# Performance work log

Measured on AMD Instinct MI355X. Metric: run time of the kernel, lower is better.

Reference implementation:

```python
import jax, jax.numpy as jnp
import numpy as np

HEAD_SIZE = 64
D_MODEL = 768


def setup_inputs() -> dict:
    key = jax.random.key(0)
    ks = jax.random.split(key, 7)
    x = jax.random.normal(ks[0], (8, 4096, D_MODEL), dtype=jnp.float32)
    def lin_init(kw, kb, fan_in, fan_out):
        bound = 1.0 / np.sqrt(fan_in)
        W = jax.random.uniform(kw, (fan_in, fan_out), minval=-bound, maxval=bound, dtype=jnp.float32)
        b = jax.random.uniform(kb, (fan_out,), minval=-bound, maxval=bound, dtype=jnp.float32)
        return W, b
    Wq, bq = lin_init(ks[1], ks[2], D_MODEL, HEAD_SIZE)
    Wk, bk = lin_init(ks[3], ks[4], D_MODEL, HEAD_SIZE)
    Wv, bv = lin_init(ks[5], ks[6], D_MODEL, HEAD_SIZE)
    return {"x": x, "Wq": Wq, "bq": bq, "Wk": Wk, "bk": bk, "Wv": Wv, "bv": bv}


def reference(x, Wq, bq, Wk, bk, Wv, bv):
    # x: [B, N, 768]; projections to [B, N, head_size]
    q = jnp.einsum("bnd,dh->bnh", x, Wq) + bq
    k = jnp.einsum("bnd,dh->bnh", x, Wk) + bk
    v = jnp.einsum("bnd,dh->bnh", x, Wv) + bv
    scale = 1.0 / jnp.sqrt(jnp.asarray(q.shape[-1], dtype=q.dtype))
    wei = jnp.einsum("bqh,bkh->bqk", q, k) * scale  # [B, N, N]
    wei = jax.nn.softmax(wei, axis=-1)
    out = jnp.einsum("bqk,bkh->bqh", wei, v)  # [B, N, head_size]
    return out
```

## Files before the change

kernel.cpp:

```cpp
#include <hip/hip_runtime.h>
#include <stdint.h>
#include <stddef.h>

typedef __bf16 bf16x8 __attribute__((ext_vector_type(8)));
typedef __bf16 bf16x4 __attribute__((ext_vector_type(4)));
typedef float  f32x4  __attribute__((ext_vector_type(4)));

#define MFMA16(A, B, C) __builtin_amdgcn_mfma_f32_16x16x32_bf16((A), (B), (C), 0, 0, 0)

#define QSCALE 0.18033688011112042f

#if __has_builtin(__builtin_amdgcn_exp2f)
__device__ __forceinline__ float fast_exp2(float x) {
    return __builtin_amdgcn_exp2f(x);
}
#else
__device__ __forceinline__ float fast_exp2(float x) {
    float r;
    asm("v_exp_f32 %0, %1" : "=v"(r) : "v"(x));
    return r;
}
#endif

__device__ __forceinline__ void async_copy16(__bf16* lds, const __bf16* g) {
    __builtin_amdgcn_global_load_lds(
        (const __attribute__((address_space(1))) void*)g,
        (__attribute__((address_space(3))) void*)lds,
        16, 0, 0);
}

__global__ __launch_bounds__(256) void qkv_proj_kernel(
    const float* __restrict__ x,
    const float* __restrict__ Wq, const float* __restrict__ bq,
    const float* __restrict__ Wk, const float* __restrict__ bk,
    const float* __restrict__ Wv, const float* __restrict__ bv,
    __bf16* __restrict__ Qg, __bf16* __restrict__ Kg, __bf16* __restrict__ Vpg)
{
    __shared__ __bf16 xs[64][40];
    __shared__ __bf16 wt[192][40];

    const int tid  = threadIdx.x;
    const int wid  = tid >> 6;
    const int lane = tid & 63;
    const int l15  = lane & 15;
    const int l4   = lane >> 4;
    const int m0   = blockIdx.x * 64;

    f32x4 acc[4][3];
    #pragma unroll
    for (int i = 0; i < 4; ++i)
        #pragma unroll
        for (int j = 0; j < 3; ++j)
            acc[i][j] = (f32x4){0.f, 0.f, 0.f, 0.f};

    for (int k0 = 0; k0 < 768; k0 += 32) {
        #pragma unroll
        for (int i = 0; i < 2; ++i) {
            int idx = tid + 256 * i;
            int row = idx >> 3;
            int c4  = idx & 7;
            const float4 v = *reinterpret_cast<const float4*>(
                x + (size_t)(m0 + row) * 768 + k0 + c4 * 4);
            bf16x4 t;
            t[0] = (__bf16)v.x; t[1] = (__bf16)v.y;
            t[2] = (__bf16)v.z; t[3] = (__bf16)v.w;
            *reinterpret_cast<bf16x4*>(&xs[row][c4 * 4]) = t;
        }
        #pragma unroll
        for (int i = 0; i < 6; ++i) {
            int idx = tid + 256 * i;
            int kg  = idx / 192;
            int c   = idx - kg * 192;
            const float* Wm = (c < 64) ? Wq : ((c < 128) ? Wk : Wv);
            int cc = c & 63;
            bf16x4 t;
            #pragma unroll
            for (int j = 0; j < 4; ++j)
                t[j] = (__bf16)Wm[(size_t)(k0 + kg * 4 + j) * 64 + cc];
            *reinterpret_cast<bf16x4*>(&wt[c][kg * 4]) = t;
        }
        __syncthreads();

        bf16x8 afrag[4];
        #pragma unroll
        for (int rf = 0; rf < 4; ++rf)
            afrag[rf] = *reinterpret_cast<const bf16x8*>(&xs[rf * 16 + l15][l4 * 8]);
        #pragma unroll
        for (int cf = 0; cf < 3; ++cf) {
            bf16x8 bfrag = *reinterpret_cast<const bf16x8*>(
                &wt[wid * 48 + cf * 16 + l15][l4 * 8]);
            #pragma unroll
            for (int rf = 0; rf < 4; ++rf)
                acc[rf][cf] = MFMA16(afrag[rf], bfrag, acc[rf][cf]);
        }
        __syncthreads();
    }

    #pragma unroll
    for (int cf = 0; cf < 3; ++cf) {
        int col = wid * 48 + cf * 16 + l15;
        int mi  = col >> 6;
        int h   = col & 63;
        float bias = (mi == 0) ? bq[h] : ((mi == 1) ? bk[h] : bv[h]);
        float scl  = (mi == 0) ? QSCALE : 1.0f;
        #pragma unroll
        for (int rf = 0; rf < 4; ++rf) {
            int r0 = rf * 16 + l4 * 4;
            if (mi == 2) {
                int m  = m0 + r0;
                int bb = m >> 12;
                int n0 = m & 4095;
                int n0p = (n0 & ~31) | (l4 * 8 + (rf & 1) * 4);
                bf16x4 t;
                #pragma unroll
                for (int r = 0; r < 4; ++r)
                    t[r] = (__bf16)(acc[rf][cf][r] + bias);
                *reinterpret_cast<bf16x4*>(
                    Vpg + ((size_t)bb * 64 + h) * 4096 + n0p) = t;
            } else {
                __bf16* G = (mi == 0) ? Qg : Kg;
                #pragma unroll
                for (int r = 0; r < 4; ++r)
                    G[(size_t)(m0 + r0 + r) * 64 + h] =
                        (__bf16)((acc[rf][cf][r] + bias) * scl);
            }
        }
    }
}

__global__ __launch_bounds__(512, 4) void attn_kernel(
    const __bf16* __restrict__ Qg, const __bf16* __restrict__ Kg,
    const __bf16* __restrict__ Vpg, float* __restrict__ out)
{
    __shared__ __align__(16) char smem[65536];
    __bf16* ksbase = reinterpret_cast<__bf16*>(smem);
    __bf16* vsbase = ksbase + 4 * 2 * 32 * 64;

    const int tid  = threadIdx.x;
    const int wid  = tid >> 6;
    const int lane = tid & 63;
    const int l15  = lane & 15;
    const int l4   = lane >> 4;
    const int qw2  = wid & 1;
    const int ks   = wid >> 1;
    const int b    = blockIdx.x & 7;
    const int qb   = blockIdx.x >> 3;
    const int q0   = qb * 64 + qw2 * 32;

    const __bf16* Kb = Kg  + (size_t)b * 4096 * 64;
    const __bf16* Vb = Vpg + (size_t)b * 64 * 4096;

    __bf16* kst0 = ksbase + (ks * 2 + 0) * 32 * 64;
    __bf16* kst1 = ksbase + (ks * 2 + 1) * 32 * 64;
    __bf16* vst0 = vsbase + (ks * 2 + 0) * 64 * 32;
    __bf16* vst1 = vsbase + (ks * 2 + 1) * 64 * 32;

    int koff[2][2], voff[4];
    #pragma unroll
    for (int dc = 0; dc < 2; ++dc)
        #pragma unroll
        for (int cf = 0; cf < 2; ++cf) {
            int row = cf * 16 + l15;
            koff[dc][cf] = row * 64 + (((dc * 4 + l4) ^ (row & 7)) * 8);
        }
    #pragma unroll
    for (int ht = 0; ht < 4; ++ht) {
        int row = ht * 16 + l15;
        voff[ht] = row * 32 + ((l4 ^ (row & 3)) * 8);
    }

    const int krow_s = qw2 * 16 + (lane >> 3);
    const int kg_s   = (lane & 7) ^ (lane >> 3);
    const int vrow_s = qw2 * 32 + (lane >> 2);
    const int vg_s   = (lane & 3) ^ ((lane >> 2) & 3);

    auto issue_stage = [&](__bf16* kp, __bf16* vp, int c) {
        #pragma unroll
        for (int j = 0; j < 2; ++j) {
            async_copy16(kp + (qw2 * 16 + j * 8) * 64,
                         Kb + (size_t)(c * 32 + krow_s + j * 8) * 64 + kg_s * 8);
            async_copy16(vp + (qw2 * 32 + j * 16) * 32,
                         Vb + (size_t)(vrow_s + j * 16) * 4096 + c * 32 + vg_s * 8);
        }
    };

    bf16x8 aq[2][2];
    #pragma unroll
    for (int set = 0; set < 2; ++set)
        #pragma unroll
        for (int dc = 0; dc < 2; ++dc)
            aq[set][dc] = *reinterpret_cast<const bf16x8*>(
                Qg + (size_t)(b * 4096 + q0 + set * 16 + l15) * 64 + dc * 32 + l4 * 8);

    f32x4 lacc0 = (f32x4){0.f, 0.f, 0.f, 0.f};
    f32x4 lacc1 = (f32x4){0.f, 0.f, 0.f, 0.f};
    f32x4 o[2][4];
    #pragma unroll
    for (int set = 0; set < 2; ++set)
        #pragma unroll
        for (int ht = 0; ht < 4; ++ht)
            o[set][ht] = (f32x4){0.f, 0.f, 0.f, 0.f};

    const int c0 = ks * 32;
    issue_stage(kst0, vst0, c0);

    for (int t = 0; t < 32; ++t) {
        __syncthreads();
        const __bf16* kp = (t & 1) ? kst1 : kst0;
        const __bf16* vp = (t & 1) ? vst1 : vst0;
        __bf16* kpn = (t & 1) ? kst0 : kst1;
        __bf16* vpn = (t & 1) ? vst0 : vst1;
        const bool pre = (t + 1) < 32;
        if (pre) issue_stage(kpn, vpn, c0 + t + 1);

        f32x4 s0[2], s1[2];
        #pragma unroll
        for (int cf = 0; cf < 2; ++cf) {
            s0[cf] = (f32x4){0.f, 0.f, 0.f, 0.f};
            s1[cf] = (f32x4){0.f, 0.f, 0.f, 0.f};
        }
        __builtin_amdgcn_s_setprio(1);
        #pragma unroll
        for (int dc = 0; dc < 2; ++dc)
            #pragma unroll
            for (int cf = 0; cf < 2; ++cf) {
                bf16x8 kf = *reinterpret_cast<const bf16x8*>(kp + koff[dc][cf]);
                s0[cf] = MFMA16(kf, aq[0][dc], s0[cf]);
                s1[cf] = MFMA16(kf, aq[1][dc], s1[cf]);
            }
        __builtin_amdgcn_s_setprio(0);

        #pragma unroll
        for (int cf = 0; cf < 2; ++cf)
            #pragma unroll
            for (int r = 0; r < 4; ++r) {
                s0[cf][r] = fast_exp2(s0[cf][r]);
                s1[cf][r] = fast_exp2(s1[cf][r]);
            }
        lacc0 += s0[0]; lacc0 += s0[1];
        lacc1 += s1[0]; lacc1 += s1[1];

        bf16x8 pb0, pb1;
        #pragma unroll
        for (int j = 0; j < 4; ++j) {
            pb0[j]     = (__bf16)s0[0][j];
            pb0[j + 4] = (__bf16)s0[1][j];
            pb1[j]     = (__bf16)s1[0][j];
            pb1[j + 4] = (__bf16)s1[1][j];
        }

        __builtin_amdgcn_s_setprio(1);
        #pragma unroll
        for (int ht = 0; ht < 4; ++ht) {
            bf16x8 vf = *reinterpret_cast<const bf16x8*>(vp + voff[ht]);
            o[0][ht] = MFMA16(vf, pb0, o[0][ht]);
            o[1][ht] = MFMA16(vf, pb1, o[1][ht]);
        }
        __builtin_amdgcn_s_setprio(0);
    }

    float l0 = lacc0[0] + lacc0[1] + lacc0[2] + lacc0[3];
    float l1 = lacc1[0] + lacc1[1] + lacc1[2] + lacc1[3];
    l0 += __shfl_xor(l0, 16); l0 += __shfl_xor(l0, 32);
    l1 += __shfl_xor(l1, 16); l1 += __shfl_xor(l1, 32);

    __syncthreads();
    float* lbuf = reinterpret_cast<float*>(smem);
    float* smO  = lbuf + 256;

    if (l4 == 0) {
        lbuf[((qw2 * 2 + 0) * 4 + ks) * 16 + l15] = l0;
        lbuf[((qw2 * 2 + 1) * 4 + ks) * 16 + l15] = l1;
    }
    const int hcol = 4 * l4;
    if (ks != 0) {
        #pragma unroll
        for (int set = 0; set < 2; ++set)
            #pragma unroll
            for (int ht = 0; ht < 4; ++ht)
                *reinterpret_cast<f32x4*>(
                    &smO[(((ks - 1) * 2 + qw2) * 32 + set * 16 + l15) * 68
                         + ht * 16 + hcol]) = o[set][ht];
    }
    __syncthreads();
    if (ks == 0) {
        #pragma unroll
        for (int set = 0; set < 2; ++set) {
            float L = lbuf[((qw2 * 2 + set) * 4 + 0) * 16 + l15]
                    + lbuf[((qw2 * 2 + set) * 4 + 1) * 16 + l15]
                    + lbuf[((qw2 * 2 + set) * 4 + 2) * 16 + l15]
                    + lbuf[((qw2 * 2 + set) * 4 + 3) * 16 + l15];
            float inv = 1.0f / L;
            #pragma unroll
            for (int ht = 0; ht < 4; ++ht) {
                f32x4 acc = o[set][ht];
                #pragma unroll
                for (int k = 1; k < 4; ++k) {
                    f32x4 p = *reinterpret_cast<const f32x4*>(
                        &smO[(((k - 1) * 2 + qw2) * 32 + set * 16 + l15) * 68
                             + ht * 16 + hcol]);
                    acc[0] += p[0]; acc[1] += p[1]; acc[2] += p[2]; acc[3] += p[3];
                }
                acc[0] *= inv; acc[1] *= inv; acc[2] *= inv; acc[3] *= inv;
                *reinterpret_cast<f32x4*>(
                    out + (size_t)(b * 4096 + q0 + set * 16 + l15) * 64
                        + ht * 16 + hcol) = acc;
            }
        }
    }
}

extern "C" void kernel_launch(void* const* d_in, const int* in_sizes, int n_in,
                              void* d_out, int out_size, void* d_ws, size_t ws_size,
                              hipStream_t stream)
{
    (void)in_sizes; (void)n_in; (void)out_size; (void)ws_size;
    const float* x  = (const float*)d_in[0];
    const float* Wq = (const float*)d_in[1];
    const float* bq = (const float*)d_in[2];
    const float* Wk = (const float*)d_in[3];
    const float* bk = (const float*)d_in[4];
    const float* Wv = (const float*)d_in[5];
    const float* bv = (const float*)d_in[6];
    float* out = (float*)d_out;

    __bf16* Qg  = (__bf16*)d_ws;
    __bf16* Kg  = Qg + (size_t)32768 * 64;
    __bf16* Vpg = Kg + (size_t)32768 * 64;

    qkv_proj_kernel<<<512, 256, 0, stream>>>(x, Wq, bq, Wk, bk, Wv, bv, Qg, Kg, Vpg);
    attn_kernel<<<512, 512, 0, stream>>>(Qg, Kg, Vpg, out);
}
```

Baseline: 75.54 us.

## Load V fragments directly from global into registers instead of LDS staging

V tiles are no longer staged through shared memory with async copies. Each lane now loads its V fragments straight from global memory into registers one iteration ahead, double-buffered in registers, and the loop is unrolled by two so the buffers can swap statically. Shared memory per block shrinks, which removes LDS traffic and bank pressure for V. In exchange it adds register pressure and relies on the global load latency being hidden within one iteration, with no coalescing help from LDS.

```diff
diff --git a/kernel.cpp b/kernel.cpp
--- a/kernel.cpp
+++ b/kernel.cpp
@@ -132,9 +132,8 @@
     const __bf16* __restrict__ Qg, const __bf16* __restrict__ Kg,
     const __bf16* __restrict__ Vpg, float* __restrict__ out)
 {
-    __shared__ __align__(16) char smem[65536];
+    __shared__ __align__(16) char smem[53248];
     __bf16* ksbase = reinterpret_cast<__bf16*>(smem);
-    __bf16* vsbase = ksbase + 4 * 2 * 32 * 64;
 
     const int tid  = threadIdx.x;
     const int wid  = tid >> 6;
@@ -152,10 +151,8 @@
 
     __bf16* kst0 = ksbase + (ks * 2 + 0) * 32 * 64;
     __bf16* kst1 = ksbase + (ks * 2 + 1) * 32 * 64;
-    __bf16* vst0 = vsbase + (ks * 2 + 0) * 64 * 32;
-    __bf16* vst1 = vsbase + (ks * 2 + 1) * 64 * 32;
-
-    int koff[2][2], voff[4];
+
+    int koff[2][2];
     #pragma unroll
     for (int dc = 0; dc < 2; ++dc)
         #pragma unroll
@@ -163,25 +160,22 @@
             int row = cf * 16 + l15;
             koff[dc][cf] = row * 64 + (((dc * 4 + l4) ^ (row & 7)) * 8);
         }
-    #pragma unroll
-    for (int ht = 0; ht < 4; ++ht) {
-        int row = ht * 16 + l15;
-        voff[ht] = row * 32 + ((l4 ^ (row & 3)) * 8);
-    }
 
     const int krow_s = qw2 * 16 + (lane >> 3);
     const int kg_s   = (lane & 7) ^ (lane >> 3);
-    const int vrow_s = qw2 * 32 + (lane >> 2);
-    const int vg_s   = (lane & 3) ^ ((lane >> 2) & 3);
-
-    auto issue_stage = [&](__bf16* kp, __bf16* vp, int c) {
-        #pragma unroll
-        for (int j = 0; j < 2; ++j) {
+
+    auto issue_stageK = [&](__bf16* kp, int c) {
+        #pragma unroll
+        for (int j = 0; j < 2; ++j)
             async_copy16(kp + (qw2 * 16 + j * 8) * 64,
                          Kb + (size_t)(c * 32 + krow_s + j * 8) * 64 + kg_s * 8);
-            async_copy16(vp + (qw2 * 32 + j * 16) * 32,
-                         Vb + (size_t)(vrow_s + j * 16) * 4096 + c * 32 + vg_s * 8);
-        }
+    };
+
+    auto vloadR = [&](bf16x8 (&dst)[4], int c) {
+        #pragma unroll
+        for (int ht = 0; ht < 4; ++ht)
+            dst[ht] = *reinterpret_cast<const bf16x8*>(
+                Vb + (size_t)(ht * 16 + l15) * 4096 + c * 32 + l4 * 8);
     };
 
     bf16x8 aq[2][2];
@@ -202,16 +196,17 @@
             o[set][ht] = (f32x4){0.f, 0.f, 0.f, 0.f};
 
     const int c0 = ks * 32;
-    issue_stage(kst0, vst0, c0);
-
-    for (int t = 0; t < 32; ++t) {
+
+    bf16x8 va[4], vb_[4];
+
+    auto body = [&](int t, const __bf16* kp, __bf16* kpn,
+                    bf16x8 (&vcur)[4], bf16x8 (&vnxt)[4]) {
         __syncthreads();
-        const __bf16* kp = (t & 1) ? kst1 : kst0;
-        const __bf16* vp = (t & 1) ? vst1 : vst0;
-        __bf16* kpn = (t & 1) ? kst0 : kst1;
-        __bf16* vpn = (t & 1) ? vst0 : vst1;
         const bool pre = (t + 1) < 32;
-        if (pre) issue_stage(kpn, vpn, c0 + t + 1);
+        if (pre) {
+            issue_stageK(kpn, c0 + t + 1);
+            vloadR(vnxt, c0 + t + 1);
+        }
 
         f32x4 s0[2], s1[2];
         #pragma unroll
@@ -224,9 +219,9 @@
         for (int dc = 0; dc < 2; ++dc)
             #pragma unroll
             for (int cf = 0; cf < 2; ++cf) {
-                bf16x8 kf = *reinterpret_cast<const bf16x8*>(kp + koff[dc][cf]);
-                s0[cf] = MFMA16(kf, aq[0][dc], s0[cf]);
-                s1[cf] = MFMA16(kf, aq[1][dc], s1[cf]);
+                bf16x8 kfr = *reinterpret_cast<const bf16x8*>(kp + koff[dc][cf]);
+                s0[cf] = MFMA16(kfr, aq[0][dc], s0[cf]);
+                s1[cf] = MFMA16(kfr, aq[1][dc], s1[cf]);
             }
         __builtin_amdgcn_s_setprio(0);
 
@@ -252,11 +247,18 @@
         __builtin_amdgcn_s_setprio(1);
         #pragma unroll
         for (int ht = 0; ht < 4; ++ht) {
-            bf16x8 vf = *reinterpret_cast<const bf16x8*>(vp + voff[ht]);
-            o[0][ht] = MFMA16(vf, pb0, o[0][ht]);
-            o[1][ht] = MFMA16(vf, pb1, o[1][ht]);
+            o[0][ht] = MFMA16(vcur[ht], pb0, o[0][ht]);
+            o[1][ht] = MFMA16(vcur[ht], pb1, o[1][ht]);
         }
         __builtin_amdgcn_s_setprio(0);
+    };
+
+    issue_stageK(kst0, c0);
+    vloadR(va, c0);
+
+    for (int j = 0; j < 16; ++j) {
+        body(2 * j,     kst0, kst1, va,  vb_);
+        body(2 * j + 1, kst1, kst0, vb_, va);
     }
 
     float l0 = lacc0[0] + lacc0[1] + lacc0[2] + lacc0[3];
```

Measured after the change: 130.6 us. 1.73x slower.

## Split attention key range across two blocks with separate merge kernel

Applied to the files above, without the earlier changes.

Splits each query tile's key range in half across two blocks, doubling the grid to 1024 blocks. Partial unnormalized outputs and row sums go to workspace, and a new merge kernel combines and normalizes them. Shared memory is halved by dropping double buffering, and the cross-wave reduction now reuses one buffer serially, so more blocks can fit per CU. In exchange it adds an extra kernel launch, global round-trips for the partials, and loses the overlap of loads with compute.

```diff
diff --git a/kernel.cpp b/kernel.cpp
--- a/kernel.cpp
+++ b/kernel.cpp
@@ -128,13 +128,14 @@
     }
 }
 
-__global__ __launch_bounds__(512, 4) void attn_kernel(
+__global__ __launch_bounds__(512, 8) void attn_kernel(
     const __bf16* __restrict__ Qg, const __bf16* __restrict__ Kg,
-    const __bf16* __restrict__ Vpg, float* __restrict__ out)
+    const __bf16* __restrict__ Vpg, float* __restrict__ po,
+    float* __restrict__ pl)
 {
-    __shared__ __align__(16) char smem[65536];
+    __shared__ __align__(16) char smem[32768];
     __bf16* ksbase = reinterpret_cast<__bf16*>(smem);
-    __bf16* vsbase = ksbase + 4 * 2 * 32 * 64;
+    __bf16* vsbase = ksbase + 4 * 32 * 64;
 
     const int tid  = threadIdx.x;
     const int wid  = tid >> 6;
@@ -144,16 +145,16 @@
     const int qw2  = wid & 1;
     const int ks   = wid >> 1;
     const int b    = blockIdx.x & 7;
-    const int qb   = blockIdx.x >> 3;
+    const int idx  = blockIdx.x >> 3;
+    const int qb   = idx & 63;
+    const int half = idx >> 6;
     const int q0   = qb * 64 + qw2 * 32;
 
     const __bf16* Kb = Kg  + (size_t)b * 4096 * 64;
     const __bf16* Vb = Vpg + (size_t)b * 64 * 4096;
 
-    __bf16* kst0 = ksbase + (ks * 2 + 0) * 32 * 64;
-    __bf16* kst1 = ksbase + (ks * 2 + 1) * 32 * 64;
-    __bf16* vst0 = vsbase + (ks * 2 + 0) * 64 * 32;
-    __bf16* vst1 = vsbase + (ks * 2 + 1) * 64 * 32;
+    __bf16* kst = ksbase + ks * 32 * 64;
+    __bf16* vst = vsbase + ks * 64 * 32;
 
     int koff[2][2], voff[4];
     #pragma unroll
@@ -174,12 +175,12 @@
     const int vrow_s = qw2 * 32 + (lane >> 2);
     const int vg_s   = (lane & 3) ^ ((lane >> 2) & 3);
 
-    auto issue_stage = [&](__bf16* kp, __bf16* vp, int c) {
+    auto issue_stage = [&](int c) {
         #pragma unroll
         for (int j = 0; j < 2; ++j) {
-            async_copy16(kp + (qw2 * 16 + j * 8) * 64,
+            async_copy16(kst + (qw2 * 16 + j * 8) * 64,
                          Kb + (size_t)(c * 32 + krow_s + j * 8) * 64 + kg_s * 8);
-            async_copy16(vp + (qw2 * 32 + j * 16) * 32,
+            async_copy16(vst + (qw2 * 32 + j * 16) * 32,
                          Vb + (size_t)(vrow_s + j * 16) * 4096 + c * 32 + vg_s * 8);
         }
     };
@@ -201,17 +202,11 @@
         for (int ht = 0; ht < 4; ++ht)
             o[set][ht] = (f32x4){0.f, 0.f, 0.f, 0.f};
 
-    const int c0 = ks * 32;
-    issue_stage(kst0, vst0, c0);
-
-    for (int t = 0; t < 32; ++t) {
-        __syncthreads();
-        const __bf16* kp = (t & 1) ? kst1 : kst0;
-        const __bf16* vp = (t & 1) ? vst1 : vst0;
-        __bf16* kpn = (t & 1) ? kst0 : kst1;
-        __bf16* vpn = (t & 1) ? vst0 : vst1;
-        const bool pre = (t + 1) < 32;
-        if (pre) issue_stage(kpn, vpn, c0 + t + 1);
+    const int c0 = half * 64 + ks * 16;
+
+    for (int t = 0; t < 16; ++t) {
+        issue_stage(c0 + t);
+        __syncthreads();
 
         f32x4 s0[2], s1[2];
         #pragma unroll
@@ -224,7 +219,7 @@
         for (int dc = 0; dc < 2; ++dc)
             #pragma unroll
             for (int cf = 0; cf < 2; ++cf) {
-                bf16x8 kf = *reinterpret_cast<const bf16x8*>(kp + koff[dc][cf]);
+                bf16x8 kf = *reinterpret_cast<const bf16x8*>(kst + koff[dc][cf]);
                 s0[cf] = MFMA16(kf, aq[0][dc], s0[cf]);
                 s1[cf] = MFMA16(kf, aq[1][dc], s1[cf]);
             }
@@ -252,11 +247,13 @@
         __builtin_amdgcn_s_setprio(1);
         #pragma unroll
         for (int ht = 0; ht < 4; ++ht) {
-            bf16x8 vf = *reinterpret_cast<const bf16x8*>(vp + voff[ht]);
+            bf16x8 vf = *reinterpret_cast<const bf16x8*>(vst + voff[ht]);
             o[0][ht] = MFMA16(vf, pb0, o[0][ht]);
             o[1][ht] = MFMA16(vf, pb1, o[1][ht]);
         }
         __builtin_amdgcn_s_setprio(0);
+
+        __syncthreads();
     }
 
     float l0 = lacc0[0] + lacc0[1] + lacc0[2] + lacc0[3];
@@ -264,50 +261,77 @@
     l0 += __shfl_xor(l0, 16); l0 += __shfl_xor(l0, 32);
     l1 += __shfl_xor(l1, 16); l1 += __shfl_xor(l1, 32);
 
-    __syncthreads();
     float* lbuf = reinterpret_cast<float*>(smem);
-    float* smO  = lbuf + 256;
+    float* smO2 = lbuf + 256;
 
     if (l4 == 0) {
         lbuf[((qw2 * 2 + 0) * 4 + ks) * 16 + l15] = l0;
         lbuf[((qw2 * 2 + 1) * 4 + ks) * 16 + l15] = l1;
     }
     const int hcol = 4 * l4;
-    if (ks != 0) {
-        #pragma unroll
-        for (int set = 0; set < 2; ++set)
+    #pragma unroll
+    for (int k = 1; k < 4; ++k) {
+        if (ks == k) {
+            #pragma unroll
+            for (int set = 0; set < 2; ++set)
+                #pragma unroll
+                for (int ht = 0; ht < 4; ++ht)
+                    *reinterpret_cast<f32x4*>(
+                        &smO2[(qw2 * 32 + set * 16 + l15) * 68 + ht * 16 + hcol]) =
+                        o[set][ht];
+        }
+        __syncthreads();
+        if (ks == 0) {
+            #pragma unroll
+            for (int set = 0; set < 2; ++set)
+                #pragma unroll
+                for (int ht = 0; ht < 4; ++ht) {
+                    f32x4 p = *reinterpret_cast<const f32x4*>(
+                        &smO2[(qw2 * 32 + set * 16 + l15) * 68 + ht * 16 + hcol]);
+                    o[set][ht][0] += p[0]; o[set][ht][1] += p[1];
+                    o[set][ht][2] += p[2]; o[set][ht][3] += p[3];
+                }
+        }
+        __syncthreads();
+    }
+
+    if (ks == 0) {
+        float* pop = po + (size_t)half * 32768 * 64;
+        #pragma unroll
+        for (int set = 0; set < 2; ++set) {
+            int row = b * 4096 + q0 + set * 16 + l15;
             #pragma unroll
             for (int ht = 0; ht < 4; ++ht)
                 *reinterpret_cast<f32x4*>(
-                    &smO[(((ks - 1) * 2 + qw2) * 32 + set * 16 + l15) * 68
-                         + ht * 16 + hcol]) = o[set][ht];
-    }
-    __syncthreads();
-    if (ks == 0) {
-        #pragma unroll
-        for (int set = 0; set < 2; ++set) {
-            float L = lbuf[((qw2 * 2 + set) * 4 + 0) * 16 + l15]
-                    + lbuf[((qw2 * 2 + set) * 4 + 1) * 16 + l15]
-                    + lbuf[((qw2 * 2 + set) * 4 + 2) * 16 + l15]
-                    + lbuf[((qw2 * 2 + set) * 4 + 3) * 16 + l15];
-            float inv = 1.0f / L;
-            #pragma unroll
-            for (int ht = 0; ht < 4; ++ht) {
-                f32x4 acc = o[set][ht];
-                #pragma unroll
-                for (int k = 1; k < 4; ++k) {
-                    f32x4 p = *reinterpret_cast<const f32x4*>(
-                        &smO[(((k - 1) * 2 + qw2) * 32 + set * 16 + l15) * 68
-                             + ht * 16 + hcol]);
-                    acc[0] += p[0]; acc[1] += p[1]; acc[2] += p[2]; acc[3] += p[3];
-                }
-                acc[0] *= inv; acc[1] *= inv; acc[2] *= inv; acc[3] *= inv;
-                *reinterpret_cast<f32x4*>(
-                    out + (size_t)(b * 4096 + q0 + set * 16 + l15) * 64
-                        + ht * 16 + hcol) = acc;
+                    pop + (size_t)row * 64 + ht * 16 + hcol) = o[set][ht];
+            if (l4 == 0) {
+                float L = lbuf[((qw2 * 2 + set) * 4 + 0) * 16 + l15]
+                        + lbuf[((qw2 * 2 + set) * 4 + 1) * 16 + l15]
+                        + lbuf[((qw2 * 2 + set) * 4 + 2) * 16 + l15]
+                        + lbuf[((qw2 * 2 + set) * 4 + 3) * 16 + l15];
+                pl[half * 32768 + row] = L;
             }
         }
     }
+}
+
+__global__ __launch_bounds__(256) void merge_kernel(
+    const float* __restrict__ po, const float* __restrict__ pl,
+    float* __restrict__ out)
+{
+    int gid = blockIdx.x * 256 + threadIdx.x;
+    int row = gid >> 4;
+    int c4  = (gid & 15) * 4;
+    float inv = 1.0f / (pl[row] + pl[32768 + row]);
+    const float4 a = *reinterpret_cast<const float4*>(po + (size_t)row * 64 + c4);
+    const float4 b = *reinterpret_cast<const float4*>(
+        po + (size_t)(32768 + row) * 64 + c4);
+    float4 r;
+    r.x = (a.x + b.x) * inv;
+    r.y = (a.y + b.y) * inv;
+    r.z = (a.z + b.z) * inv;
+    r.w = (a.w + b.w) * inv;
+    *reinterpret_cast<float4*>(out + (size_t)row * 64 + c4) = r;
 }
 
 extern "C" void kernel_launch(void* const* d_in, const int* in_sizes, int n_in,
@@ -327,7 +351,10 @@
     __bf16* Qg  = (__bf16*)d_ws;
     __bf16* Kg  = Qg + (size_t)32768 * 64;
     __bf16* Vpg = Kg + (size_t)32768 * 64;
+    float*  po  = (float*)(Vpg + (size_t)32768 * 64);
+    float*  pl  = po + (size_t)2 * 32768 * 64;
 
     qkv_proj_kernel<<<512, 256, 0, stream>>>(x, Wq, bq, Wk, bk, Wv, bv, Qg, Kg, Vpg);
-    attn_kernel<<<512, 512, 0, stream>>>(Qg, Kg, Vpg, out);
-}
+    attn_kernel<<<1024, 512, 0, stream>>>(Qg, Kg, Vpg, po, pl);
+    merge_kernel<<<2048, 256, 0, stream>>>(po, pl, out);
+}
```

Result: slower. 243.6 us (+222.5%).

## Give each wave all 64 queries and split keys eight ways with tree reduction

Applied to the files above, without the earlier changes.

Each wave now covers all 64 queries of the block instead of 32, and the key range is split across eight waves instead of four. Every K/V fragment read from LDS therefore feeds four MFMAs instead of two, which cuts LDS read traffic per unit of math. Each wave also copies whole 32-key stages on its own. The partial outputs are combined with a three-level tree reduction through LDS. In exchange, LDS use doubles to 128 KB per block and per-wave registers grow, so fewer blocks can be resident per CU and latency hiding may suffer.

```diff
diff --git a/kernel.cpp b/kernel.cpp
--- a/kernel.cpp
+++ b/kernel.cpp
@@ -128,24 +128,23 @@
     }
 }
 
-__global__ __launch_bounds__(512, 4) void attn_kernel(
+__global__ __launch_bounds__(512, 2) void attn_kernel(
     const __bf16* __restrict__ Qg, const __bf16* __restrict__ Kg,
     const __bf16* __restrict__ Vpg, float* __restrict__ out)
 {
-    __shared__ __align__(16) char smem[65536];
+    __shared__ __align__(16) char smem[131072];
     __bf16* ksbase = reinterpret_cast<__bf16*>(smem);
-    __bf16* vsbase = ksbase + 4 * 2 * 32 * 64;
+    __bf16* vsbase = ksbase + 8 * 2 * 32 * 64;
 
     const int tid  = threadIdx.x;
     const int wid  = tid >> 6;
     const int lane = tid & 63;
     const int l15  = lane & 15;
     const int l4   = lane >> 4;
-    const int qw2  = wid & 1;
-    const int ks   = wid >> 1;
+    const int ks   = wid;
     const int b    = blockIdx.x & 7;
-    const int qb   = blockIdx.x >> 3;
-    const int q0   = qb * 64 + qw2 * 32;
+    const int qt   = blockIdx.x >> 3;
+    const int q0   = qt * 64;
 
     const __bf16* Kb = Kg  + (size_t)b * 4096 * 64;
     const __bf16* Vb = Vpg + (size_t)b * 64 * 4096;
@@ -169,142 +168,167 @@
         voff[ht] = row * 32 + ((l4 ^ (row & 3)) * 8);
     }
 
-    const int krow_s = qw2 * 16 + (lane >> 3);
-    const int kg_s   = (lane & 7) ^ (lane >> 3);
-    const int vrow_s = qw2 * 32 + (lane >> 2);
-    const int vg_s   = (lane & 3) ^ ((lane >> 2) & 3);
+    const int krow = lane >> 3;
+    const int kg_s = (lane & 7) ^ (lane >> 3);
+    const int vrow = lane >> 2;
+    const int vg_s = (lane & 3) ^ ((lane >> 2) & 3);
 
     auto issue_stage = [&](__bf16* kp, __bf16* vp, int c) {
         #pragma unroll
-        for (int j = 0; j < 2; ++j) {
-            async_copy16(kp + (qw2 * 16 + j * 8) * 64,
-                         Kb + (size_t)(c * 32 + krow_s + j * 8) * 64 + kg_s * 8);
-            async_copy16(vp + (qw2 * 32 + j * 16) * 32,
-                         Vb + (size_t)(vrow_s + j * 16) * 4096 + c * 32 + vg_s * 8);
+        for (int j = 0; j < 4; ++j) {
+            async_copy16(kp + j * 8 * 64,
+                         Kb + (size_t)(c * 32 + j * 8 + krow) * 64 + kg_s * 8);
+            async_copy16(vp + j * 16 * 32,
+                         Vb + (size_t)(j * 16 + vrow) * 4096 + c * 32 + vg_s * 8);
         }
     };
 
-    bf16x8 aq[2][2];
-    #pragma unroll
-    for (int set = 0; set < 2; ++set)
+    bf16x8 aq[4][2];
+    #pragma unroll
+    for (int set = 0; set < 4; ++set)
         #pragma unroll
         for (int dc = 0; dc < 2; ++dc)
             aq[set][dc] = *reinterpret_cast<const bf16x8*>(
                 Qg + (size_t)(b * 4096 + q0 + set * 16 + l15) * 64 + dc * 32 + l4 * 8);
 
-    f32x4 lacc0 = (f32x4){0.f, 0.f, 0.f, 0.f};
-    f32x4 lacc1 = (f32x4){0.f, 0.f, 0.f, 0.f};
-    f32x4 o[2][4];
-    #pragma unroll
-    for (int set = 0; set < 2; ++set)
+    f32x4 lacc[4];
+    f32x4 o[4][4];
+    #pragma unroll
+    for (int set = 0; set < 4; ++set) {
+        lacc[set] = (f32x4){0.f, 0.f, 0.f, 0.f};
         #pragma unroll
         for (int ht = 0; ht < 4; ++ht)
             o[set][ht] = (f32x4){0.f, 0.f, 0.f, 0.f};
-
-    const int c0 = ks * 32;
+    }
+
+    const int c0 = ks * 16;
     issue_stage(kst0, vst0, c0);
 
-    for (int t = 0; t < 32; ++t) {
+    for (int t = 0; t < 16; ++t) {
         __syncthreads();
         const __bf16* kp = (t & 1) ? kst1 : kst0;
         const __bf16* vp = (t & 1) ? vst1 : vst0;
         __bf16* kpn = (t & 1) ? kst0 : kst1;
         __bf16* vpn = (t & 1) ? vst0 : vst1;
-        const bool pre = (t + 1) < 32;
+        const bool pre = (t + 1) < 16;
         if (pre) issue_stage(kpn, vpn, c0 + t + 1);
 
-        f32x4 s0[2], s1[2];
-        #pragma unroll
-        for (int cf = 0; cf < 2; ++cf) {
-            s0[cf] = (f32x4){0.f, 0.f, 0.f, 0.f};
-            s1[cf] = (f32x4){0.f, 0.f, 0.f, 0.f};
-        }
+        f32x4 s[4][2];
+        #pragma unroll
+        for (int set = 0; set < 4; ++set)
+            #pragma unroll
+            for (int cf = 0; cf < 2; ++cf)
+                s[set][cf] = (f32x4){0.f, 0.f, 0.f, 0.f};
         __builtin_amdgcn_s_setprio(1);
         #pragma unroll
         for (int dc = 0; dc < 2; ++dc)
             #pragma unroll
             for (int cf = 0; cf < 2; ++cf) {
                 bf16x8 kf = *reinterpret_cast<const bf16x8*>(kp + koff[dc][cf]);
-                s0[cf] = MFMA16(kf, aq[0][dc], s0[cf]);
-                s1[cf] = MFMA16(kf, aq[1][dc], s1[cf]);
+                #pragma unroll
+                for (int set = 0; set < 4; ++set)
+                    s[set][cf] = MFMA16(kf, aq[set][dc], s[set][cf]);
             }
         __builtin_amdgcn_s_setprio(0);
 
         #pragma unroll
-        for (int cf = 0; cf < 2; ++cf)
-            #pragma unroll
-            for (int r = 0; r < 4; ++r) {
-                s0[cf][r] = fast_exp2(s0[cf][r]);
-                s1[cf][r] = fast_exp2(s1[cf][r]);
-            }
-        lacc0 += s0[0]; lacc0 += s0[1];
-        lacc1 += s1[0]; lacc1 += s1[1];
-
-        bf16x8 pb0, pb1;
-        #pragma unroll
-        for (int j = 0; j < 4; ++j) {
-            pb0[j]     = (__bf16)s0[0][j];
-            pb0[j + 4] = (__bf16)s0[1][j];
-            pb1[j]     = (__bf16)s1[0][j];
-            pb1[j + 4] = (__bf16)s1[1][j];
-        }
+        for (int set = 0; set < 4; ++set) {
+            #pragma unroll
+            for (int cf = 0; cf < 2; ++cf)
+                #pragma unroll
+                for (int r = 0; r < 4; ++r)
+                    s[set][cf][r] = fast_exp2(s[set][cf][r]);
+            lacc[set] += s[set][0];
+            lacc[set] += s[set][1];
+        }
+
+        bf16x8 pb[4];
+        #pragma unroll
+        for (int set = 0; set < 4; ++set)
+            #pragma unroll
+            for (int j = 0; j < 4; ++j) {
+                pb[set][j]     = (__bf16)s[set][0][j];
+                pb[set][j + 4] = (__bf16)s[set][1][j];
+            }
 
         __builtin_amdgcn_s_setprio(1);
         #pragma unroll
         for (int ht = 0; ht < 4; ++ht) {
             bf16x8 vf = *reinterpret_cast<const bf16x8*>(vp + voff[ht]);
-            o[0][ht] = MFMA16(vf, pb0, o[0][ht]);
-            o[1][ht] = MFMA16(vf, pb1, o[1][ht]);
+            #pragma unroll
+            for (int set = 0; set < 4; ++set)
+                o[set][ht] = MFMA16(vf, pb[set], o[set][ht]);
         }
         __builtin_amdgcn_s_setprio(0);
     }
 
-    float l0 = lacc0[0] + lacc0[1] + lacc0[2] + lacc0[3];
-    float l1 = lacc1[0] + lacc1[1] + lacc1[2] + lacc1[3];
-    l0 += __shfl_xor(l0, 16); l0 += __shfl_xor(l0, 32);
-    l1 += __shfl_xor(l1, 16); l1 += __shfl_xor(l1, 32);
+    float lw[4];
+    #pragma unroll
+    for (int set = 0; set < 4; ++set) {
+        float v = lacc[set][0] + lacc[set][1] + lacc[set][2] + lacc[set][3];
+        v += __shfl_xor(v, 16);
+        v += __shfl_xor(v, 32);
+        lw[set] = v;
+    }
 
     __syncthreads();
     float* lbuf = reinterpret_cast<float*>(smem);
-    float* smO  = lbuf + 256;
+    float* obuf = lbuf + 512;
+    const int hcol = 4 * l4;
 
     if (l4 == 0) {
-        lbuf[((qw2 * 2 + 0) * 4 + ks) * 16 + l15] = l0;
-        lbuf[((qw2 * 2 + 1) * 4 + ks) * 16 + l15] = l1;
-    }
-    const int hcol = 4 * l4;
-    if (ks != 0) {
-        #pragma unroll
-        for (int set = 0; set < 2; ++set)
+        #pragma unroll
+        for (int set = 0; set < 4; ++set)
+            lbuf[ks * 64 + set * 16 + l15] = lw[set];
+    }
+
+    auto writeO = [&](int bufi) {
+        #pragma unroll
+        for (int set = 0; set < 4; ++set)
             #pragma unroll
             for (int ht = 0; ht < 4; ++ht)
                 *reinterpret_cast<f32x4*>(
-                    &smO[(((ks - 1) * 2 + qw2) * 32 + set * 16 + l15) * 68
-                         + ht * 16 + hcol]) = o[set][ht];
-    }
+                    &obuf[bufi * 4352 + (set * 16 + l15) * 68 + ht * 16 + hcol]) =
+                    o[set][ht];
+    };
+    auto addO = [&](int bufi) {
+        #pragma unroll
+        for (int set = 0; set < 4; ++set)
+            #pragma unroll
+            for (int ht = 0; ht < 4; ++ht) {
+                f32x4 p = *reinterpret_cast<const f32x4*>(
+                    &obuf[bufi * 4352 + (set * 16 + l15) * 68 + ht * 16 + hcol]);
+                o[set][ht][0] += p[0]; o[set][ht][1] += p[1];
+                o[set][ht][2] += p[2]; o[set][ht][3] += p[3];
+            }
+    };
+
+    if (ks >= 4) writeO(ks - 4);
+    __syncthreads();
+    if (ks < 4) addO(ks);
+    __syncthreads();
+    if (ks == 2 || ks == 3) writeO(ks - 2);
+    __syncthreads();
+    if (ks < 2) addO(ks);
+    __syncthreads();
+    if (ks == 1) writeO(0);
     __syncthreads();
     if (ks == 0) {
-        #pragma unroll
-        for (int set = 0; set < 2; ++set) {
-            float L = lbuf[((qw2 * 2 + set) * 4 + 0) * 16 + l15]
-                    + lbuf[((qw2 * 2 + set) * 4 + 1) * 16 + l15]
-                    + lbuf[((qw2 * 2 + set) * 4 + 2) * 16 + l15]
-                    + lbuf[((qw2 * 2 + set) * 4 + 3) * 16 + l15];
+        addO(0);
+        #pragma unroll
+        for (int set = 0; set < 4; ++set) {
+            int q = set * 16 + l15;
+            float L = 0.f;
+            #pragma unroll
+            for (int k = 0; k < 8; ++k)
+                L += lbuf[k * 64 + q];
             float inv = 1.0f / L;
             #pragma unroll
             for (int ht = 0; ht < 4; ++ht) {
                 f32x4 acc = o[set][ht];
-                #pragma unroll
-                for (int k = 1; k < 4; ++k) {
-                    f32x4 p = *reinterpret_cast<const f32x4*>(
-                        &smO[(((k - 1) * 2 + qw2) * 32 + set * 16 + l15) * 68
-                             + ht * 16 + hcol]);
-                    acc[0] += p[0]; acc[1] += p[1]; acc[2] += p[2]; acc[3] += p[3];
-                }
                 acc[0] *= inv; acc[1] *= inv; acc[2] *= inv; acc[3] *= inv;
                 *reinterpret_cast<f32x4*>(
-                    out + (size_t)(b * 4096 + q0 + set * 16 + l15) * 64
-                        + ht * 16 + hcol) = acc;
+                    out + (size_t)(b * 4096 + q0 + q) * 64 + ht * 16 + hcol) = acc;
             }
         }
     }
```

Result: slower. 83.10 us (+10.0%).
